# Kernel tuning notes

Hardware: AMD Instinct MI355X
Metric: run time of the kernel (lower is better)

Reference implementation:

```python
import jax, jax.numpy as jnp
import numpy as np
from jax import lax

B, C, H, W = 8, 512, 64, 64
COUT, K = 512, 3
STYLE_DIM = 512


def setup_inputs() -> dict:
    key = jax.random.key(0)
    k1, k2, k3, k4, k5 = jax.random.split(key, 5)
    x = jax.random.normal(k1, (B, C, H, W), dtype=jnp.float32)
    style = jax.random.normal(k2, (B, STYLE_DIM), dtype=jnp.float32)
    # conv weight (OIHW), scaled like a typical init
    weight = jax.random.normal(k3, (COUT, C, K, K), dtype=jnp.float32) * (1.0 / np.sqrt(C * K * K))
    # modulation Linear: style_dim -> in_channels
    mod_w = jax.random.normal(k4, (C, STYLE_DIM), dtype=jnp.float32) * (1.0 / np.sqrt(STYLE_DIM))
    mod_b = jnp.ones((C,), dtype=jnp.float32) + 0.01 * jax.random.normal(k5, (C,), dtype=jnp.float32)
    return {"x": x, "style": style, "weight": weight, "mod_w": mod_w, "mod_b": mod_b}


def reference(x, style, weight, mod_w, mod_b):
    # s = modulation(style): Linear, shape (B, C) -> per-sample per-channel scale
    s = style @ mod_w.T + mod_b  # (B, C)
    xm = x * s[:, :, None, None]  # modulate input (B, C, H, W)
    # The torch code runs conv2d(groups=B) with weight.repeat(B,1,1,1); since the
    # weight is identical per group this equals a plain batched conv.
    y = lax.conv_general_dilated(
        xm, weight,
        window_strides=(1, 1),
        padding=[(1, 1), (1, 1)],
        rhs_dilation=(1, 1),
        dimension_numbers=("NCHW", "OIHW", "NCHW"),
    )  # (B, COUT, H, W)
    return y
```

## Files before the change

### kernel.cpp

```cpp
#include <hip/hip_runtime.h>
#include <cstdint>
#include <cstddef>

typedef short s16x8 __attribute__((ext_vector_type(8)));
typedef float f32x16 __attribute__((ext_vector_type(16)));

#define WS_S     0
#define WS_ZERO  16384
#define WS_XQ    32768
#define XQ_BYTES (8 * 64 * 64 * 64 * 16)
#define WS_WQ    (WS_XQ + XQ_BYTES)
#define WQ_BYTES (4 * 32 * 9 * 2 * 128 * 8 * 2)
#define WS_NEEDED ((size_t)WS_WQ + (size_t)WQ_BYTES)

__device__ __forceinline__ short f2bf(float f) {
  unsigned u = __builtin_bit_cast(unsigned, f);
  unsigned r = (u + 0x7fffu + ((u >> 16) & 1u)) >> 16;
  return (short)r;
}

__device__ __forceinline__ void gload_lds16(const void* g, void* l) {
  __builtin_amdgcn_global_load_lds(
      (const __attribute__((address_space(1))) void*)g,
      (__attribute__((address_space(3))) void*)l, 16, 0, 0);
}

__global__ void k_style(const float* __restrict__ style,
                        const float* __restrict__ mod_w,
                        const float* __restrict__ mod_b,
                        float* __restrict__ s_out,
                        float* __restrict__ zb) {
  if (blockIdx.x == 0) zb[threadIdx.x] = 0.0f;
  int wave = threadIdx.x >> 6, lane = threadIdx.x & 63;
  int wid = blockIdx.x * 4 + wave;
  int b = wid >> 9, c = wid & 511;
  const float4* st = (const float4*)(style + b * 512);
  const float4* mw = (const float4*)(mod_w + c * 512);
  float4 a0 = st[lane * 2], a1 = st[lane * 2 + 1];
  float4 b0 = mw[lane * 2], b1 = mw[lane * 2 + 1];
  float sum = a0.x * b0.x + a0.y * b0.y + a0.z * b0.z + a0.w * b0.w +
              a1.x * b1.x + a1.y * b1.y + a1.z * b1.z + a1.w * b1.w;
  #pragma unroll
  for (int off = 32; off; off >>= 1) sum += __shfl_down(sum, off);
  if (lane == 0) s_out[b * 512 + c] = sum + mod_b[c];
}

__global__ void k_xq(const float* __restrict__ x, const float* __restrict__ s,
                     char* __restrict__ xq) {
  int t = blockIdx.x * 256 + threadIdx.x;
  int w = t & 63, cg = (t >> 6) & 63, h = (t >> 12) & 63, b = t >> 18;
  const float* xp = x + (((b * 512 + cg * 8) * 64 + h) * 64 + w);
  const float* sp = s + b * 512 + cg * 8;
  s16x8 v;
  #pragma unroll
  for (int j = 0; j < 8; ++j) v[j] = f2bf(xp[j * 4096] * sp[j]);
  *(s16x8*)(xq + (size_t)t * 16) = v;
}

__global__ void k_wq(const float* __restrict__ wt, char* __restrict__ wq) {
  int tap = blockIdx.x, ch = blockIdx.y, nb = blockIdx.z;
  int kg = threadIdx.x >> 7, n = threadIdx.x & 127;
  const float* wp = wt + ((size_t)(nb * 128 + n) * 512 + ch * 16 + kg * 8) * 9 + tap;
  s16x8 v;
  #pragma unroll
  for (int j = 0; j < 8; ++j) v[j] = f2bf(wp[j * 9]);
  size_t idx = ((size_t)(nb * 32 + ch) * 9 + tap) * 256 + kg * 128 + n;
  *(s16x8*)(wq + idx * 16) = v;
}

__global__ __launch_bounds__(512, 2) void k_conv(
    const char* __restrict__ xq, const char* __restrict__ wq,
    const char* __restrict__ zerob, float* __restrict__ out) {
  extern __shared__ char smem[];
  char* wt_base = smem;
  char* xs_base = smem + 73728;

  const int tid = threadIdx.x;
  const int lane = tid & 63, wave = tid >> 6;
  const int l5 = lane >> 5, l31 = lane & 31;
  const int wc = wave >> 2;
  const int wp = wave & 3;
  const int wrot = wave % 3;
  const int mb = blockIdx.x, nb = blockIdx.y;
  const int b = mb >> 3;
  const int row0 = (mb & 7) << 3;

  if (tid < 80) {
    int dbuf = tid / 40, q = tid % 40;
    int j = q >> 2, kg = (q >> 1) & 1, side = q & 1;
    s16x8 z = {0, 0, 0, 0, 0, 0, 0, 0};
    *(s16x8*)(xs_base + dbuf * 21120 + ((j * 2 + kg) * 66 + side * 65) * 16) = z;
  }

  f32x16 acc[2][4];
  #pragma unroll
  for (int i = 0; i < 2; ++i)
    #pragma unroll
    for (int j = 0; j < 4; ++j)
      #pragma unroll
      for (int e = 0; e < 16; ++e) acc[i][j][e] = 0.0f;

  const char* wq_base = wq + (size_t)nb * (32 * 36864) + lane * 16;
  const char* xq_base = xq + (size_t)b * 4194304 + lane * 16;

  const int a_off = l5 * 2048 + l31 * 16;
  const int b_off = l5 * 1056 + l31 * 16;
  const int xs_woff = wp * 4224;

  #define STAGE(buf, ch)                                                      \
    _Pragma("unroll")                                                         \
    for (int i = 0; i < 7; ++i) {                                             \
      int seg = wave * 7 + i;                        \
      if (seg < 36) {                                                         \
        gload_lds16(wq_base + (size_t)(ch) * 36864 + seg * 1024,              \
                    wt_base + (buf) * 36864 + seg * 1024);                    \
      } else {                                                                \
        int q = seg - 36, j = q >> 1, kg = q & 1;                             \
        int h = row0 - 1 + j;                                                 \
        const char* src = (h >= 0 && h < 64)                                  \
            ? xq_base + (size_t)(h * 64 + (ch) * 2 + kg) * 1024               \
            : zerob + lane * 16;                                              \
        gload_lds16(src, xs_base + (buf) * 21120 + ((j * 2 + kg) * 66 + 1) * 16); \
      }                                                                       \
    }

  STAGE(0, 0);
  __syncthreads();

  for (int ch = 0; ch < 32; ++ch) {
    const int cur = ch & 1;
    if (ch < 31) STAGE(cur ^ 1, ch + 1);

    const char* wt = wt_base + cur * 36864;
    const char* xs_w = xs_base + cur * 21120 + xs_woff;

    #pragma unroll
    for (int kwi = 0; kwi < 3; ++kwi) {
      const int kw = (kwi + wrot) % 3;
      s16x8 bC[4][2];
      #pragma unroll
      for (int r4 = 0; r4 < 4; ++r4)
        #pragma unroll
        for (int chh = 0; chh < 2; ++chh)
          bC[r4][chh] = *(const s16x8*)(xs_w + (r4 * 132 + chh * 32 + kw) * 16 + b_off);
      #pragma unroll
      for (int kh = 0; kh < 3; ++kh) {
        const int tap = kh * 3 + kw;
        s16x8 afr[2];
        #pragma unroll
        for (int ct = 0; ct < 2; ++ct)
          afr[ct] = *(const s16x8*)(wt + tap * 4096 + (wc * 2 + ct) * 512 + a_off);
        __builtin_amdgcn_s_setprio(1);
        #pragma unroll
        for (int ct = 0; ct < 2; ++ct)
          #pragma unroll
          for (int pt = 0; pt < 4; ++pt)
            acc[ct][pt] = __builtin_amdgcn_mfma_f32_32x32x16_bf16(
                afr[ct], bC[(pt >> 1) + kh][pt & 1], acc[ct][pt], 0, 0, 0);
        __builtin_amdgcn_s_setprio(0);
      }
    }
    __syncthreads();
  }

  #pragma unroll
  for (int ct = 0; ct < 2; ++ct) {
    #pragma unroll
    for (int pt = 0; pt < 4; ++pt) {
      int h = row0 + wp * 2 + (pt >> 1);
      int w = (pt & 1) * 32 + l31;
      int cb = nb * 128 + wc * 64 + ct * 32 + 4 * l5;
      #pragma unroll
      for (int rg = 0; rg < 16; ++rg) {
        int cout = cb + (rg & 3) + 8 * (rg >> 2);
        out[((size_t)(b * 512 + cout) * 4096) + h * 64 + w] = acc[ct][pt][rg];
      }
    }
  }
  #undef STAGE
}

__global__ void k_naive(const float* __restrict__ x, const float* __restrict__ style,
                        const float* __restrict__ wt, const float* __restrict__ mw,
                        const float* __restrict__ mb_, float* __restrict__ out) {
  __shared__ float s_sh[512];
  int h = blockIdx.x, co = blockIdx.y, b = blockIdx.z, w = threadIdx.x;
  for (int c = w; c < 512; c += 64) {
    float a = mb_[c];
    for (int k = 0; k < 512; ++k) a += style[b * 512 + k] * mw[c * 512 + k];
    s_sh[c] = a;
  }
  __syncthreads();
  float acc = 0.0f;
  for (int c = 0; c < 512; ++c) {
    float sc = s_sh[c];
    const float* wp = wt + ((size_t)co * 512 + c) * 9;
    for (int kh = 0; kh < 3; ++kh) {
      int hy = h + kh - 1;
      if (hy < 0 || hy >= 64) continue;
      for (int kw = 0; kw < 3; ++kw) {
        int wx = w + kw - 1;
        if (wx < 0 || wx >= 64) continue;
        acc += wp[kh * 3 + kw] * x[((size_t)(b * 512 + c) * 64 + hy) * 64 + wx] * sc;
      }
    }
  }
  out[((size_t)(b * 512 + co) * 64 + h) * 64 + w] = acc;
}

extern "C" void kernel_launch(void* const* d_in, const int* in_sizes, int n_in,
                              void* d_out, int out_size, void* d_ws, size_t ws_size,
                              hipStream_t stream) {
  const float* x      = (const float*)d_in[0];
  const float* style  = (const float*)d_in[1];
  const float* weight = (const float*)d_in[2];
  const float* mod_w  = (const float*)d_in[3];
  const float* mod_b  = (const float*)d_in[4];
  float* out = (float*)d_out;
  char* ws = (char*)d_ws;

  if (ws_size >= WS_NEEDED) {
    float* s  = (float*)(ws + WS_S);
    float* zb = (float*)(ws + WS_ZERO);
    char* xq  = ws + WS_XQ;
    char* wq  = ws + WS_WQ;
    k_style<<<1024, 256, 0, stream>>>(style, mod_w, mod_b, s, zb);
    k_xq<<<8192, 256, 0, stream>>>(x, s, xq);
    k_wq<<<dim3(9, 32, 4), 256, 0, stream>>>(weight, wq);
    k_conv<<<dim3(64, 4), 512, 115968, stream>>>(xq, wq, (const char*)zb, out);
  } else {
    k_naive<<<dim3(64, 512, 8), 64, 0, stream>>>(x, style, weight, mod_w, mod_b, out);
  }
}
```

Measured before the change: 157.0 us.

## Load conv weight fragments directly from global memory instead of staging through LDS

Removes the weight tile from LDS staging: each wave now reads its A fragments straight from the pre-packed global weight buffer with a three-slot register prefetch ring across the nine taps. Shared memory drops from about 113 KB to about 41 KB per block, which lowers LDS traffic and may allow more resident blocks. In exchange, weight reads go through L2/global latency inside the MFMA loop and are no longer shared across waves. The per-wave kw rotation is also dropped.

```diff
diff --git a/kernel.cpp b/kernel.cpp
--- a/kernel.cpp
+++ b/kernel.cpp
@@ -72,15 +72,13 @@
     const char* __restrict__ xq, const char* __restrict__ wq,
     const char* __restrict__ zerob, float* __restrict__ out) {
   extern __shared__ char smem[];
-  char* wt_base = smem;
-  char* xs_base = smem + 73728;
+  char* xs_base = smem;
 
   const int tid = threadIdx.x;
   const int lane = tid & 63, wave = tid >> 6;
   const int l5 = lane >> 5, l31 = lane & 31;
   const int wc = wave >> 2;
   const int wp = wave & 3;
-  const int wrot = wave % 3;
   const int mb = blockIdx.x, nb = blockIdx.y;
   const int b = mb >> 3;
   const int row0 = (mb & 7) << 3;
@@ -100,22 +98,18 @@
       #pragma unroll
       for (int e = 0; e < 16; ++e) acc[i][j][e] = 0.0f;
 
-  const char* wq_base = wq + (size_t)nb * (32 * 36864) + lane * 16;
   const char* xq_base = xq + (size_t)b * 4194304 + lane * 16;
-
-  const int a_off = l5 * 2048 + l31 * 16;
+  const char* wqa = wq + (size_t)nb * 1179648 + l5 * 2048 + (wc * 64 + l31) * 16;
+
   const int b_off = l5 * 1056 + l31 * 16;
   const int xs_woff = wp * 4224;
 
   #define STAGE(buf, ch)                                                      \
     _Pragma("unroll")                                                         \
-    for (int i = 0; i < 7; ++i) {                                             \
-      int seg = wave * 7 + i;                        \
-      if (seg < 36) {                                                         \
-        gload_lds16(wq_base + (size_t)(ch) * 36864 + seg * 1024,              \
-                    wt_base + (buf) * 36864 + seg * 1024);                    \
-      } else {                                                                \
-        int q = seg - 36, j = q >> 1, kg = q & 1;                             \
+    for (int i = 0; i < 3; ++i) {                                             \
+      int seg = wave * 3 + i;                               \
+      if (seg < 20) {                                                         \
+        int j = seg >> 1, kg = seg & 1;                                       \
         int h = row0 - 1 + j;                                                 \
         const char* src = (h >= 0 && h < 64)                                  \
             ? xq_base + (size_t)(h * 64 + (ch) * 2 + kg) * 1024               \
@@ -124,41 +118,46 @@
       }                                                                       \
     }
 
+  #define LOAD_A(slot, clv)                                                   \
+    { const int kw_ = (clv) / 3, kh_ = (clv) % 3, tap_ = kh_ * 3 + kw_;       \
+      ap[slot][0] = *(const s16x8*)(wqc + tap_ * 4096 + 0 * 512);             \
+      ap[slot][1] = *(const s16x8*)(wqc + tap_ * 4096 + 1 * 512); }
+
   STAGE(0, 0);
   __syncthreads();
+
+  s16x8 ap[3][2];
+  s16x8 bC[4][2];
 
   for (int ch = 0; ch < 32; ++ch) {
     const int cur = ch & 1;
     if (ch < 31) STAGE(cur ^ 1, ch + 1);
 
-    const char* wt = wt_base + cur * 36864;
+    const char* wqc = wqa + (size_t)ch * 36864;
     const char* xs_w = xs_base + cur * 21120 + xs_woff;
 
+    LOAD_A(0, 0);
+    LOAD_A(1, 1);
+
     #pragma unroll
-    for (int kwi = 0; kwi < 3; ++kwi) {
-      const int kw = (kwi + wrot) % 3;
-      s16x8 bC[4][2];
+    for (int cl = 0; cl < 9; ++cl) {
+      const int kw = cl / 3, kh = cl % 3;
+      if (cl < 7) LOAD_A((cl + 2) % 3, cl + 2);
+      if (kh == 0) {
+        #pragma unroll
+        for (int r4 = 0; r4 < 4; ++r4)
+          #pragma unroll
+          for (int chh = 0; chh < 2; ++chh)
+            bC[r4][chh] = *(const s16x8*)(xs_w + (r4 * 132 + chh * 32 + kw) * 16 + b_off);
+      }
+      __builtin_amdgcn_s_setprio(1);
       #pragma unroll
-      for (int r4 = 0; r4 < 4; ++r4)
+      for (int ct = 0; ct < 2; ++ct)
         #pragma unroll
-        for (int chh = 0; chh < 2; ++chh)
-          bC[r4][chh] = *(const s16x8*)(xs_w + (r4 * 132 + chh * 32 + kw) * 16 + b_off);
-      #pragma unroll
-      for (int kh = 0; kh < 3; ++kh) {
-        const int tap = kh * 3 + kw;
-        s16x8 afr[2];
-        #pragma unroll
-        for (int ct = 0; ct < 2; ++ct)
-          afr[ct] = *(const s16x8*)(wt + tap * 4096 + (wc * 2 + ct) * 512 + a_off);
-        __builtin_amdgcn_s_setprio(1);
-        #pragma unroll
-        for (int ct = 0; ct < 2; ++ct)
-          #pragma unroll
-          for (int pt = 0; pt < 4; ++pt)
-            acc[ct][pt] = __builtin_amdgcn_mfma_f32_32x32x16_bf16(
-                afr[ct], bC[(pt >> 1) + kh][pt & 1], acc[ct][pt], 0, 0, 0);
-        __builtin_amdgcn_s_setprio(0);
-      }
+        for (int pt = 0; pt < 4; ++pt)
+          acc[ct][pt] = __builtin_amdgcn_mfma_f32_32x32x16_bf16(
+              ap[cl % 3][ct], bC[(pt >> 1) + kh][pt & 1], acc[ct][pt], 0, 0, 0);
+      __builtin_amdgcn_s_setprio(0);
     }
     __syncthreads();
   }
@@ -178,6 +177,7 @@
     }
   }
   #undef STAGE
+  #undef LOAD_A
 }
 
 __global__ void k_naive(const float* __restrict__ x, const float* __restrict__ style,
@@ -227,7 +227,7 @@
     k_style<<<1024, 256, 0, stream>>>(style, mod_w, mod_b, s, zb);
     k_xq<<<8192, 256, 0, stream>>>(x, s, xq);
     k_wq<<<dim3(9, 32, 4), 256, 0, stream>>>(weight, wq);
-    k_conv<<<dim3(64, 4), 512, 115968, stream>>>(xq, wq, (const char*)zb, out);
+    k_conv<<<dim3(64, 4), 512, 42240, stream>>>(xq, wq, (const char*)zb, out);
   } else {
     k_naive<<<dim3(64, 512, 8), 64, 0, stream>>>(x, style, weight, mod_w, mod_b, out);
   }
```

After: 169.6 us. 1.08x slower.
